# Kernel optimization log

Measured on AMD Instinct MI355X. Metric: run time of the kernel, lower is better.

## Reference

```python
import jax, jax.numpy as jnp
import numpy as np

N = 3000          # num_sample (nodes)
N_OMICS = 3000    # input feature dims for both omics
ENC1, ENC2, NZ = 256, 128, 64


def _xavier(key, fan_in, fan_out):
    limit = float(np.sqrt(6.0 / (fan_in + fan_out)))
    return jax.random.uniform(key, (fan_in, fan_out), jnp.float32, -limit, limit)


def setup_inputs() -> dict:
    key = jax.random.key(0)
    ks = jax.random.split(key, 20)
    inp = {
        "omics_1": jax.random.normal(ks[0], (N, N_OMICS), jnp.float32),
        "omics_2": jax.random.normal(ks[1], (N, N_OMICS), jnp.float32),
    }
    # random dense adjacency, row-normalized (as a typical normalized graph operator)
    for i, name in enumerate(["adj_feature_omics1", "adj_feature_omics2",
                              "adj_spatial_omics1", "adj_spatial_omics2"]):
        a = jax.random.uniform(ks[2 + i], (N, N), jnp.float32)
        inp[name] = a / jnp.sum(a, axis=1, keepdims=True)
    # GNNLayer weights for the four GAE encoders (xavier uniform, as in reset_parameters)
    dims = [(N_OMICS, ENC1), (ENC1, ENC2), (ENC2, NZ)]
    kidx = 6
    for enc in ["f1", "f2", "s1", "s2"]:
        for li, (fi, fo) in enumerate(dims, start=1):
            inp[f"w_{enc}_{li}"] = _xavier(ks[kidx], fi, fo)
            kidx += 1
    return inp


def _gae_encoder(x, adj, w1, w2, w3):
    # GNNLayer: support = act(x @ W); out = spmm(adj, support). Dropout is identity (eval).
    z = adj @ jnp.tanh(x @ w1)          # [N, ENC1]
    z = adj @ jnp.tanh(z @ w2)          # [N, ENC2]
    z = adj @ (z @ w3)                  # [N, NZ]  (no activation on layer 3)
    adj_hat = jax.nn.sigmoid(z @ z.T)   # [N, N]
    return z, adj_hat


def reference(omics_1, omics_2,
              adj_feature_omics1, adj_feature_omics2,
              adj_spatial_omics1, adj_spatial_omics2,
              w_f1_1, w_f1_2, w_f1_3,
              w_f2_1, w_f2_2, w_f2_3,
              w_s1_1, w_s1_2, w_s1_3,
              w_s2_1, w_s2_2, w_s2_3):
    _, a1 = _gae_encoder(omics_1, adj_feature_omics1, w_f1_1, w_f1_2, w_f1_3)
    _, a2 = _gae_encoder(omics_2, adj_feature_omics2, w_f2_1, w_f2_2, w_f2_3)
    _, a3 = _gae_encoder(omics_1, adj_spatial_omics1, w_s1_1, w_s1_2, w_s1_3)
    _, a4 = _gae_encoder(omics_2, adj_spatial_omics2, w_s2_1, w_s2_2, w_s2_3)
    # stacked reconstructed adjacencies from the four encoders [4, N, N]
    return jnp.stack([a1, a2, a3, a4], axis=0)
```

## Files before the change

kernel.cpp:

```cpp
#include <hip/hip_runtime.h>
#include <stdint.h>
#include <stddef.h>


typedef __attribute__((ext_vector_type(8))) _Float16 half8;
typedef __attribute__((ext_vector_type(4))) float f32x4;

#define PAD 3072
#define MR  3000
#define ADJ_STRIDE ((size_t)PAD * PAD)

static __device__ __forceinline__ void async_cp16(const _Float16* g, _Float16* l) {
    __builtin_amdgcn_global_load_lds((const __attribute__((address_space(1))) void*)g,
                                     (__attribute__((address_space(3))) void*)l, 16, 0, 0);
}

struct Adj4 { const float* src[4]; };

__global__ __launch_bounds__(256) void adj_cast4(Adj4 p, _Float16* __restrict__ dst) {
    const int z   = blockIdx.y;
    const int idx = blockIdx.x * 256 + threadIdx.x;
    const int row = idx / 192;
    const int u   = idx - row * 192;
    const int c0  = u * 16;
    const float* sp = p.src[z] + (size_t)row * MR + c0;
    _Float16* d = dst + (size_t)z * ADJ_STRIDE + (size_t)row * PAD + c0;
    half8 h0, h1;
    const bool rok = row < MR;
    if (rok && c0 < MR) {
        f32x4 v0 = __builtin_nontemporal_load((const f32x4*)sp);
        f32x4 v1 = __builtin_nontemporal_load((const f32x4*)(sp + 4));
        #pragma unroll
        for (int j = 0; j < 4; ++j) { h0[j] = (_Float16)v0[j]; h0[4 + j] = (_Float16)v1[j]; }
    } else {
        #pragma unroll
        for (int j = 0; j < 8; ++j) h0[j] = (_Float16)0.f;
    }
    if (rok && c0 + 8 < MR) {
        f32x4 v2 = __builtin_nontemporal_load((const f32x4*)(sp + 8));
        f32x4 v3 = __builtin_nontemporal_load((const f32x4*)(sp + 12));
        #pragma unroll
        for (int j = 0; j < 4; ++j) { h1[j] = (_Float16)v2[j]; h1[4 + j] = (_Float16)v3[j]; }
    } else {
        #pragma unroll
        for (int j = 0; j < 8; ++j) h1[j] = (_Float16)0.f;
    }
    *(half8*)d = h0;
    *(half8*)(d + 8) = h1;
}

struct Wt12 { const float* src[12]; _Float16* dst[12];
              int fi[12]; int fo[12]; int ldk[12]; int nr[12]; };

__global__ __launch_bounds__(256) void wt_cast12(Wt12 p) {
    const int z   = blockIdx.y;
    const int idx = blockIdx.x * 256 + threadIdx.x;
    const int ldk = p.ldk[z];
    if (idx >= p.nr[z] * ldk) return;
    const int r = idx / ldk;
    const int k = idx - r * ldk;
    float v = 0.f;
    if (r < p.fo[z] && k < p.fi[z]) v = p.src[z][(size_t)k * p.fo[z] + r];
    p.dst[z][(size_t)r * ldk + k] = (_Float16)v;
}

template<int ACT, int OMODE, int S, int BSRC>
__global__ __launch_bounds__(256, 2)
void gemm_bt(const _Float16* __restrict__ Aall, size_t aStride,
             const _Float16* __restrict__ Ball, size_t bStride,
             const float* __restrict__ Bf0, const float* __restrict__ Bf1,
             void* __restrict__ Call, size_t cStride,
             int M, int Ncols, int Kp, int lda, int ldb, int ldc,
             int mBound, int nBound)
{
    __shared__ _Float16 smem[128 * 64 * 2];
    _Float16* As = smem;
    _Float16* Bs = smem + 8192;

    const int z   = blockIdx.z;
    const int e   = z / S;
    const int ksl = z - e * S;
    const int Kslice = Kp / S;
    const int kbase  = ksl * Kslice;

    const _Float16* A = Aall + (size_t)e * aStride;
    const _Float16* B = Ball + (size_t)e * bStride;
    const float*    Bf = (e & 1) ? Bf1 : Bf0;

    const int tm = blockIdx.x * 128;
    const int tn = blockIdx.y * 128;
    const int t    = threadIdx.x;
    const int lane = t & 63;
    const int w    = t >> 6;
    const int wm   = (w >> 1) * 64;
    const int wn   = (w & 1) * 64;
    const int lr   = lane & 15;
    const int lg   = lane >> 4;

    f32x4 acc[4][4];
    const f32x4 zero = {0.f, 0.f, 0.f, 0.f};
    #pragma unroll
    for (int i = 0; i < 4; ++i)
        #pragma unroll
        for (int j = 0; j < 4; ++j) acc[i][j] = zero;

    const int nkt = Kslice >> 6;
    for (int kt = 0; kt < nkt; ++kt) {
        const int k0 = kbase + (kt << 6);
        #pragma unroll
        for (int i = 0; i < 4; ++i) {
            const int c = t + i * 256;
            const int row = c >> 3, slot = c & 7;
            const int ss = slot ^ (row & 7);
            async_cp16(A + (size_t)(tm + row) * lda + k0 + ss * 8, &As[c * 8]);
        }
        if (BSRC) {
            #pragma unroll
            for (int i = 0; i < 4; ++i) {
                const int c = t + i * 256;
                const int row = c >> 3, g = c & 7;
                const int grow = tn + row;
                const int gcol = k0 + g * 8;
                half8 h;
                if (grow < MR && gcol < MR) {
                    const float* bp = Bf + (size_t)grow * MR + gcol;
                    f32x4 v0 = *(const f32x4*)bp;
                    f32x4 v1 = *(const f32x4*)(bp + 4);
                    #pragma unroll
                    for (int j = 0; j < 4; ++j) { h[j] = (_Float16)v0[j]; h[4 + j] = (_Float16)v1[j]; }
                } else {
                    #pragma unroll
                    for (int j = 0; j < 8; ++j) h[j] = (_Float16)0.f;
                }
                *(half8*)&Bs[row * 64 + ((g ^ (row & 7)) << 3)] = h;
            }
        } else {
            #pragma unroll
            for (int i = 0; i < 4; ++i) {
                const int c = t + i * 256;
                const int row = c >> 3, slot = c & 7;
                const int ss = slot ^ (row & 7);
                async_cp16(B + (size_t)(tn + row) * ldb + k0 + ss * 8, &Bs[c * 8]);
            }
        }
        __syncthreads();

        #pragma unroll
        for (int ks = 0; ks < 2; ++ks) {
            half8 af[4], bf[4];
            #pragma unroll
            for (int mi = 0; mi < 4; ++mi) {
                const int ra = wm + mi * 16 + lr;
                const int s  = (ks * 4 + lg) ^ (ra & 7);
                af[mi] = *(const half8*)((const char*)As + ra * 128 + s * 16);
            }
            #pragma unroll
            for (int ni = 0; ni < 4; ++ni) {
                const int rb = wn + ni * 16 + lr;
                const int s  = (ks * 4 + lg) ^ (rb & 7);
                bf[ni] = *(const half8*)((const char*)Bs + rb * 128 + s * 16);
            }
            #pragma unroll
            for (int mi = 0; mi < 4; ++mi)
                #pragma unroll
                for (int ni = 0; ni < 4; ++ni)
                    acc[mi][ni] = __builtin_amdgcn_mfma_f32_16x16x32_f16(
                        af[mi], bf[ni], acc[mi][ni], 0, 0, 0);
        }
        __syncthreads();
    }

    if (OMODE == 0) {
        _Float16* C = (_Float16*)Call + (size_t)e * cStride;
        #pragma unroll
        for (int mi = 0; mi < 4; ++mi)
            #pragma unroll
            for (int rr = 0; rr < 4; ++rr) {
                const int m = tm + wm + mi * 16 + lg * 4 + rr;
                #pragma unroll
                for (int ni = 0; ni < 4; ++ni) {
                    const int n = tn + wn + ni * 16 + lr;
                    float x = acc[mi][ni][rr];
                    if (ACT) x = tanhf(x);
                    const bool ok = (m < M) && (n < Ncols);
                    C[(size_t)m * ldc + n] = ok ? (_Float16)x : (_Float16)0.f;
                }
            }
    } else {
        float* Cp = (float*)Call +
                    (size_t)(OMODE == 3 ? z : e) * cStride;
        float* ep = (float*)smem + w * 2048;
        #pragma unroll
        for (int hs = 0; hs < 2; ++hs) {
            __syncthreads();
            #pragma unroll
            for (int mi2 = 0; mi2 < 2; ++mi2)
                #pragma unroll
                for (int ni = 0; ni < 4; ++ni)
                    #pragma unroll
                    for (int rr = 0; rr < 4; ++rr) {
                        const int row = mi2 * 16 + lg * 4 + rr;
                        const int col = ni * 16 + lr;
                        const int sw  = (((row ^ (row >> 2)) & 3) << 4);
                        ep[row * 64 + (col ^ sw)] = acc[hs * 2 + mi2][ni][rr];
                    }
            __syncthreads();
            #pragma unroll
            for (int r2 = 0; r2 < 8; ++r2) {
                const int row = r2 * 4 + (lane >> 4);
                const int c4  = (lane & 15) * 4;
                const int sw  = (((row ^ (row >> 2)) & 3) << 4);
                f32x4 v = *(const f32x4*)&ep[row * 64 + (c4 ^ sw)];
                const int gm = tm + wm + hs * 32 + row;
                const int gn = tn + wn + c4;
                if (gm < mBound && gn < nBound) {
                    if (OMODE == 2) {
                        #pragma unroll
                        for (int j = 0; j < 4; ++j)
                            v[j] = 1.0f / (1.0f + __expf(-v[j]));
                    }
                    *(f32x4*)&Cp[(size_t)gm * ldc + gn] = v;
                }
            }
        }
    }
}

template<int ACT, int S>
__global__ __launch_bounds__(256)
void reduce_k(const float* __restrict__ P, _Float16* __restrict__ out, size_t region)
{
    const size_t e    = blockIdx.y;
    const size_t base = (size_t)(blockIdx.x * 256 + threadIdx.x) * 8;
    const float* p0 = P + e * S * region + base;
    f32x4 s0 = {0.f, 0.f, 0.f, 0.f}, s1 = s0;
    #pragma unroll
    for (int s = 0; s < S; ++s) {
        const float* p = p0 + (size_t)s * region;
        s0 += *(const f32x4*)p;
        s1 += *(const f32x4*)(p + 4);
    }
    half8 h;
    #pragma unroll
    for (int j = 0; j < 8; ++j) {
        float x = (j < 4) ? s0[j] : s1[j - 4];
        if (ACT) x = tanhf(x);
        h[j] = (_Float16)x;
    }
    *(half8*)(out + e * region + base) = h;
}

extern "C" void kernel_launch(void* const* d_in, const int* in_sizes, int n_in,
                              void* d_out, int out_size, void* d_ws, size_t ws_size,
                              hipStream_t stream)
{
    const float* X1 = (const float*)d_in[0];
    const float* X2 = (const float*)d_in[1];

    const size_t R1 = 786432;
    const size_t R2 = 393216;

    float* Part = (float*)d_ws;
    _Float16* hb = (_Float16*)(Part + 16 * R2);
    size_t off = 0;
    auto alloc = [&](size_t elems) { _Float16* p = hb + off; off += elems; return p; };
    _Float16* T1  = alloc(4 * R1);
    _Float16* Z1  = alloc(4 * R1);
    _Float16* T2  = alloc(4 * R2);
    _Float16* Z2  = alloc(4 * R2);
    _Float16* T3  = alloc(4 * R2);
    _Float16* Z3  = alloc(4 * R2);
    _Float16* W1t = alloc(4ull * 256 * PAD);
    _Float16* W2t = alloc(4ull * 128 * 256);
    _Float16* W3t = alloc(4ull * 128 * 128);
    _Float16* Adj = (_Float16*)d_out;

    Adj4 a4;
    for (int i = 0; i < 4; ++i) a4.src[i] = (const float*)d_in[2 + i];
    adj_cast4<<<dim3(2304, 4, 1), 256, 0, stream>>>(a4, Adj);

    Wt12 w12;
    for (int enc = 0; enc < 4; ++enc) {
        w12.src[enc]     = (const float*)d_in[6 + enc * 3 + 0];
        w12.dst[enc]     = W1t + (size_t)enc * 256 * PAD;
        w12.fi[enc] = MR;  w12.fo[enc] = 256; w12.ldk[enc] = PAD; w12.nr[enc] = 256;

        w12.src[4 + enc] = (const float*)d_in[6 + enc * 3 + 1];
        w12.dst[4 + enc] = W2t + (size_t)enc * 128 * 256;
        w12.fi[4 + enc] = 256; w12.fo[4 + enc] = 128; w12.ldk[4 + enc] = 256; w12.nr[4 + enc] = 128;

        w12.src[8 + enc] = (const float*)d_in[6 + enc * 3 + 2];
        w12.dst[8 + enc] = W3t + (size_t)enc * 128 * 128;
        w12.fi[8 + enc] = 128; w12.fo[8 + enc] = 64; w12.ldk[8 + enc] = 128; w12.nr[8 + enc] = 128;
    }
    wt_cast12<<<dim3(3072, 12, 1), 256, 0, stream>>>(w12);

    const int BIG = 1 << 30;

    gemm_bt<0, 3, 2, 1><<<dim3(2, 24, 8), 256, 0, stream>>>(
        W1t, (size_t)256 * PAD, nullptr, 0, X1, X2,
        Part, R1, 256, PAD, PAD, PAD, MR, PAD, BIG, BIG);
    reduce_k<1, 2><<<dim3(384, 4, 1), 256, 0, stream>>>(Part, T1, R1);

    gemm_bt<0, 3, 2, 0><<<dim3(24, 2, 8), 256, 0, stream>>>(
        Adj, ADJ_STRIDE, T1, R1, nullptr, nullptr,
        Part, R1, PAD, 256, PAD, PAD, PAD, 256, BIG, BIG);
    reduce_k<0, 2><<<dim3(384, 4, 1), 256, 0, stream>>>(Part, Z1, R1);

    gemm_bt<0, 3, 2, 0><<<dim3(1, 24, 8), 256, 0, stream>>>(
        W2t, (size_t)128 * 256, Z1, R1, nullptr, nullptr,
        Part, R2, 128, PAD, 256, 256, 256, PAD, BIG, BIG);
    reduce_k<1, 2><<<dim3(192, 4, 1), 256, 0, stream>>>(Part, T2, R2);

    gemm_bt<0, 3, 4, 0><<<dim3(24, 1, 16), 256, 0, stream>>>(
        Adj, ADJ_STRIDE, T2, R2, nullptr, nullptr,
        Part, R2, PAD, 128, PAD, PAD, PAD, 128, BIG, BIG);
    reduce_k<0, 4><<<dim3(192, 4, 1), 256, 0, stream>>>(Part, Z2, R2);

    gemm_bt<0, 0, 1, 0><<<dim3(1, 24, 4), 256, 0, stream>>>(
        W3t, (size_t)128 * 128, Z2, R2, nullptr, nullptr,
        T3, R2, 128, PAD, 128, 128, 128, PAD, BIG, BIG);

    gemm_bt<0, 3, 4, 0><<<dim3(24, 1, 16), 256, 0, stream>>>(
        Adj, ADJ_STRIDE, T3, R2, nullptr, nullptr,
        Part, R2, PAD, 128, PAD, PAD, PAD, 128, BIG, BIG);
    reduce_k<0, 4><<<dim3(192, 4, 1), 256, 0, stream>>>(Part, Z3, R2);

    gemm_bt<0, 2, 1, 0><<<dim3(24, 24, 4), 256, 0, stream>>>(
        Z3, R2, Z3, R2, nullptr, nullptr,
        d_out, (size_t)MR * MR, MR, MR, 128, 128, 128, MR, MR, MR);
}
```

Measured before the change: 312.1 us.

## Fuse adjacency cast into first GEMM launch, raise split-K, halve final K

The adjacency fp32-to-fp16 cast now runs as extra blocks inside the same launch as the first X·W1 GEMM, so the bandwidth-bound cast overlaps with compute instead of running as a separate kernel. Split-K factors rise (2→4 for the first two GEMMs, 4→8 for the two adjacency×128-wide GEMMs) to put more blocks on the device. The final Z·Zᵀ GEMM uses K=64 instead of the padded 128. The split-K partial buffer moves into the unused tail of the output buffer. The extra split-K slices add partial-sum traffic and reduction work in exchange for better occupancy.

New measurement: 274.4 us. -12.1%, faster.

```diff
diff --git a/kernel.cpp b/kernel.cpp
--- a/kernel.cpp
+++ b/kernel.cpp
@@ -13,40 +13,6 @@
 static __device__ __forceinline__ void async_cp16(const _Float16* g, _Float16* l) {
     __builtin_amdgcn_global_load_lds((const __attribute__((address_space(1))) void*)g,
                                      (__attribute__((address_space(3))) void*)l, 16, 0, 0);
-}
-
-struct Adj4 { const float* src[4]; };
-
-__global__ __launch_bounds__(256) void adj_cast4(Adj4 p, _Float16* __restrict__ dst) {
-    const int z   = blockIdx.y;
-    const int idx = blockIdx.x * 256 + threadIdx.x;
-    const int row = idx / 192;
-    const int u   = idx - row * 192;
-    const int c0  = u * 16;
-    const float* sp = p.src[z] + (size_t)row * MR + c0;
-    _Float16* d = dst + (size_t)z * ADJ_STRIDE + (size_t)row * PAD + c0;
-    half8 h0, h1;
-    const bool rok = row < MR;
-    if (rok && c0 < MR) {
-        f32x4 v0 = __builtin_nontemporal_load((const f32x4*)sp);
-        f32x4 v1 = __builtin_nontemporal_load((const f32x4*)(sp + 4));
-        #pragma unroll
-        for (int j = 0; j < 4; ++j) { h0[j] = (_Float16)v0[j]; h0[4 + j] = (_Float16)v1[j]; }
-    } else {
-        #pragma unroll
-        for (int j = 0; j < 8; ++j) h0[j] = (_Float16)0.f;
-    }
-    if (rok && c0 + 8 < MR) {
-        f32x4 v2 = __builtin_nontemporal_load((const f32x4*)(sp + 8));
-        f32x4 v3 = __builtin_nontemporal_load((const f32x4*)(sp + 12));
-        #pragma unroll
-        for (int j = 0; j < 4; ++j) { h1[j] = (_Float16)v2[j]; h1[4 + j] = (_Float16)v3[j]; }
-    } else {
-        #pragma unroll
-        for (int j = 0; j < 8; ++j) h1[j] = (_Float16)0.f;
-    }
-    *(half8*)d = h0;
-    *(half8*)(d + 8) = h1;
 }
 
 struct Wt12 { const float* src[12]; _Float16* dst[12];
@@ -64,31 +30,33 @@
     p.dst[z][(size_t)r * ldk + k] = (_Float16)v;
 }
 
+struct GArgs {
+    const _Float16* Aall; size_t aStride;
+    const _Float16* Ball; size_t bStride;
+    const float* Bf0; const float* Bf1;
+    void* Call; size_t cStride;
+    int M, Ncols, Kp, lda, ldb, ldc, mBound, nBound;
+};
+
 template<int ACT, int OMODE, int S, int BSRC>
-__global__ __launch_bounds__(256, 2)
-void gemm_bt(const _Float16* __restrict__ Aall, size_t aStride,
-             const _Float16* __restrict__ Ball, size_t bStride,
-             const float* __restrict__ Bf0, const float* __restrict__ Bf1,
-             void* __restrict__ Call, size_t cStride,
-             int M, int Ncols, int Kp, int lda, int ldb, int ldc,
-             int mBound, int nBound)
+static __device__ __forceinline__
+void gemm_body(const GArgs& ga, int bx, int by, int bz, _Float16* smem)
 {
-    __shared__ _Float16 smem[128 * 64 * 2];
     _Float16* As = smem;
     _Float16* Bs = smem + 8192;
 
-    const int z   = blockIdx.z;
+    const int z   = bz;
     const int e   = z / S;
     const int ksl = z - e * S;
-    const int Kslice = Kp / S;
+    const int Kslice = ga.Kp / S;
     const int kbase  = ksl * Kslice;
 
-    const _Float16* A = Aall + (size_t)e * aStride;
-    const _Float16* B = Ball + (size_t)e * bStride;
-    const float*    Bf = (e & 1) ? Bf1 : Bf0;
-
-    const int tm = blockIdx.x * 128;
-    const int tn = blockIdx.y * 128;
+    const _Float16* A = ga.Aall + (size_t)e * ga.aStride;
+    const _Float16* B = ga.Ball + (size_t)e * ga.bStride;
+    const float*    Bf = (e & 1) ? ga.Bf1 : ga.Bf0;
+
+    const int tm = bx * 128;
+    const int tn = by * 128;
     const int t    = threadIdx.x;
     const int lane = t & 63;
     const int w    = t >> 6;
@@ -112,7 +80,7 @@
             const int c = t + i * 256;
             const int row = c >> 3, slot = c & 7;
             const int ss = slot ^ (row & 7);
-            async_cp16(A + (size_t)(tm + row) * lda + k0 + ss * 8, &As[c * 8]);
+            async_cp16(A + (size_t)(tm + row) * ga.lda + k0 + ss * 8, &As[c * 8]);
         }
         if (BSRC) {
             #pragma unroll
@@ -140,7 +108,7 @@
                 const int c = t + i * 256;
                 const int row = c >> 3, slot = c & 7;
                 const int ss = slot ^ (row & 7);
-                async_cp16(B + (size_t)(tn + row) * ldb + k0 + ss * 8, &Bs[c * 8]);
+                async_cp16(B + (size_t)(tn + row) * ga.ldb + k0 + ss * 8, &Bs[c * 8]);
             }
         }
         __syncthreads();
@@ -171,7 +139,7 @@
     }
 
     if (OMODE == 0) {
-        _Float16* C = (_Float16*)Call + (size_t)e * cStride;
+        _Float16* C = (_Float16*)ga.Call + (size_t)e * ga.cStride;
         #pragma unroll
         for (int mi = 0; mi < 4; ++mi)
             #pragma unroll
@@ -182,13 +150,12 @@
                     const int n = tn + wn + ni * 16 + lr;
                     float x = acc[mi][ni][rr];
                     if (ACT) x = tanhf(x);
-                    const bool ok = (m < M) && (n < Ncols);
-                    C[(size_t)m * ldc + n] = ok ? (_Float16)x : (_Float16)0.f;
+                    const bool ok = (m < ga.M) && (n < ga.Ncols);
+                    C[(size_t)m * ga.ldc + n] = ok ? (_Float16)x : (_Float16)0.f;
                 }
             }
     } else {
-        float* Cp = (float*)Call +
-                    (size_t)(OMODE == 3 ? z : e) * cStride;
+        float* Cp = (float*)ga.Call + (size_t)(OMODE == 3 ? z : e) * ga.cStride;
         float* ep = (float*)smem + w * 2048;
         #pragma unroll
         for (int hs = 0; hs < 2; ++hs) {
@@ -213,16 +180,68 @@
                 f32x4 v = *(const f32x4*)&ep[row * 64 + (c4 ^ sw)];
                 const int gm = tm + wm + hs * 32 + row;
                 const int gn = tn + wn + c4;
-                if (gm < mBound && gn < nBound) {
+                if (gm < ga.mBound && gn < ga.nBound) {
                     if (OMODE == 2) {
                         #pragma unroll
                         for (int j = 0; j < 4; ++j)
                             v[j] = 1.0f / (1.0f + __expf(-v[j]));
                     }
-                    *(f32x4*)&Cp[(size_t)gm * ldc + gn] = v;
+                    *(f32x4*)&Cp[(size_t)gm * ga.ldc + gn] = v;
                 }
             }
         }
+    }
+}
+
+template<int ACT, int OMODE, int S, int BSRC>
+__global__ __launch_bounds__(256, 2)
+void gemm_bt(GArgs ga) {
+    __shared__ _Float16 smem[16384];
+    gemm_body<ACT, OMODE, S, BSRC>(ga, blockIdx.x, blockIdx.y, blockIdx.z, smem);
+}
+
+struct Adj4 { const float* src[4]; };
+
+__global__ __launch_bounds__(256, 2)
+void fused_s1(GArgs ga, Adj4 a4, _Float16* __restrict__ adst)
+{
+    __shared__ _Float16 smem[16384];
+    const int b = blockIdx.x;
+    if (b < 768) {
+        const int bz = b & 15;
+        const int r  = b >> 4;
+        gemm_body<0, 3, 4, 1>(ga, r & 1, r >> 1, bz, smem);
+    } else {
+        const int cb  = b - 768;
+        const int zz  = cb / 2304;
+        const int idx = (cb - zz * 2304) * 256 + threadIdx.x;
+        const int row = idx / 192;
+        const int u   = idx - row * 192;
+        const int c0  = u * 16;
+        const float* sp = a4.src[zz] + (size_t)row * MR + c0;
+        _Float16* d = adst + (size_t)zz * ADJ_STRIDE + (size_t)row * PAD + c0;
+        half8 h0, h1;
+        const bool rok = row < MR;
+        if (rok && c0 < MR) {
+            f32x4 v0 = __builtin_nontemporal_load((const f32x4*)sp);
+            f32x4 v1 = __builtin_nontemporal_load((const f32x4*)(sp + 4));
+            #pragma unroll
+            for (int j = 0; j < 4; ++j) { h0[j] = (_Float16)v0[j]; h0[4 + j] = (_Float16)v1[j]; }
+        } else {
+            #pragma unroll
+            for (int j = 0; j < 8; ++j) h0[j] = (_Float16)0.f;
+        }
+        if (rok && c0 + 8 < MR) {
+            f32x4 v2 = __builtin_nontemporal_load((const f32x4*)(sp + 8));
+            f32x4 v3 = __builtin_nontemporal_load((const f32x4*)(sp + 12));
+            #pragma unroll
+            for (int j = 0; j < 4; ++j) { h1[j] = (_Float16)v2[j]; h1[4 + j] = (_Float16)v3[j]; }
+        } else {
+            #pragma unroll
+            for (int j = 0; j < 8; ++j) h1[j] = (_Float16)0.f;
+        }
+        *(half8*)d = h0;
+        *(half8*)(d + 8) = h1;
     }
 }
 
@@ -260,8 +279,10 @@
     const size_t R1 = 786432;
     const size_t R2 = 393216;
 
-    float* Part = (float*)d_ws;
-    _Float16* hb = (_Float16*)(Part + 16 * R2);
+    _Float16* Adj  = (_Float16*)d_out;
+    float*    Part = (float*)(Adj + 4 * ADJ_STRIDE);
+
+    _Float16* hb = (_Float16*)d_ws;
     size_t off = 0;
     auto alloc = [&](size_t elems) { _Float16* p = hb + off; off += elems; return p; };
     _Float16* T1  = alloc(4 * R1);
@@ -273,11 +294,6 @@
     _Float16* W1t = alloc(4ull * 256 * PAD);
     _Float16* W2t = alloc(4ull * 128 * 256);
     _Float16* W3t = alloc(4ull * 128 * 128);
-    _Float16* Adj = (_Float16*)d_out;
-
-    Adj4 a4;
-    for (int i = 0; i < 4; ++i) a4.src[i] = (const float*)d_in[2 + i];
-    adj_cast4<<<dim3(2304, 4, 1), 256, 0, stream>>>(a4, Adj);
 
     Wt12 w12;
     for (int enc = 0; enc < 4; ++enc) {
@@ -297,36 +313,38 @@
 
     const int BIG = 1 << 30;
 
-    gemm_bt<0, 3, 2, 1><<<dim3(2, 24, 8), 256, 0, stream>>>(
-        W1t, (size_t)256 * PAD, nullptr, 0, X1, X2,
-        Part, R1, 256, PAD, PAD, PAD, MR, PAD, BIG, BIG);
-    reduce_k<1, 2><<<dim3(384, 4, 1), 256, 0, stream>>>(Part, T1, R1);
-
-    gemm_bt<0, 3, 2, 0><<<dim3(24, 2, 8), 256, 0, stream>>>(
-        Adj, ADJ_STRIDE, T1, R1, nullptr, nullptr,
-        Part, R1, PAD, 256, PAD, PAD, PAD, 256, BIG, BIG);
-    reduce_k<0, 2><<<dim3(384, 4, 1), 256, 0, stream>>>(Part, Z1, R1);
-
-    gemm_bt<0, 3, 2, 0><<<dim3(1, 24, 8), 256, 0, stream>>>(
-        W2t, (size_t)128 * 256, Z1, R1, nullptr, nullptr,
-        Part, R2, 128, PAD, 256, 256, 256, PAD, BIG, BIG);
+    GArgs g1 = { W1t, (size_t)256 * PAD, nullptr, 0, X1, X2,
+                 Part, R1, 256, PAD, PAD, PAD, MR, PAD, BIG, BIG };
+    Adj4 a4;
+    for (int i = 0; i < 4; ++i) a4.src[i] = (const float*)d_in[2 + i];
+    fused_s1<<<dim3(9984, 1, 1), 256, 0, stream>>>(g1, a4, Adj);
+    reduce_k<1, 4><<<dim3(384, 4, 1), 256, 0, stream>>>(Part, T1, R1);
+
+    GArgs g2 = { Adj, ADJ_STRIDE, T1, R1, nullptr, nullptr,
+                 Part, R1, PAD, 256, PAD, PAD, PAD, 256, BIG, BIG };
+    gemm_bt<0, 3, 4, 0><<<dim3(24, 2, 16), 256, 0, stream>>>(g2);
+    reduce_k<0, 4><<<dim3(384, 4, 1), 256, 0, stream>>>(Part, Z1, R1);
+
+    GArgs g3 = { W2t, (size_t)128 * 256, Z1, R1, nullptr, nullptr,
+                 Part, R2, 128, PAD, 256, 256, 256, PAD, BIG, BIG };
+    gemm_bt<0, 3, 2, 0><<<dim3(1, 24, 8), 256, 0, stream>>>(g3);
     reduce_k<1, 2><<<dim3(192, 4, 1), 256, 0, stream>>>(Part, T2, R2);
 
-    gemm_bt<0, 3, 4, 0><<<dim3(24, 1, 16), 256, 0, stream>>>(
-        Adj, ADJ_STRIDE, T2, R2, nullptr, nullptr,
-        Part, R2, PAD, 128, PAD, PAD, PAD, 128, BIG, BIG);
-    reduce_k<0, 4><<<dim3(192, 4, 1), 256, 0, stream>>>(Part, Z2, R2);
-
-    gemm_bt<0, 0, 1, 0><<<dim3(1, 24, 4), 256, 0, stream>>>(
-        W3t, (size_t)128 * 128, Z2, R2, nullptr, nullptr,
-        T3, R2, 128, PAD, 128, 128, 128, PAD, BIG, BIG);
-
-    gemm_bt<0, 3, 4, 0><<<dim3(24, 1, 16), 256, 0, stream>>>(
-        Adj, ADJ_STRIDE, T3, R2, nullptr, nullptr,
-        Part, R2, PAD, 128, PAD, PAD, PAD, 128, BIG, BIG);
-    reduce_k<0, 4><<<dim3(192, 4, 1), 256, 0, stream>>>(Part, Z3, R2);
-
-    gemm_bt<0, 2, 1, 0><<<dim3(24, 24, 4), 256, 0, stream>>>(
-        Z3, R2, Z3, R2, nullptr, nullptr,
-        d_out, (size_t)MR * MR, MR, MR, 128, 128, 128, MR, MR, MR);
-}
+    GArgs g4 = { Adj, ADJ_STRIDE, T2, R2, nullptr, nullptr,
+                 Part, R2, PAD, 128, PAD, PAD, PAD, 128, BIG, BIG };
+    gemm_bt<0, 3, 8, 0><<<dim3(24, 1, 32), 256, 0, stream>>>(g4);
+    reduce_k<0, 8><<<dim3(192, 4, 1), 256, 0, stream>>>(Part, Z2, R2);
+
+    GArgs g5 = { W3t, (size_t)128 * 128, Z2, R2, nullptr, nullptr,
+                 T3, R2, 128, PAD, 128, 128, 128, PAD, BIG, BIG };
+    gemm_bt<0, 0, 1, 0><<<dim3(1, 24, 4), 256, 0, stream>>>(g5);
+
+    GArgs g6 = { Adj, ADJ_STRIDE, T3, R2, nullptr, nullptr,
+                 Part, R2, PAD, 128, PAD, PAD, PAD, 128, BIG, BIG };
+    gemm_bt<0, 3, 8, 0><<<dim3(24, 1, 32), 256, 0, stream>>>(g6);
+    reduce_k<0, 8><<<dim3(192, 4, 1), 256, 0, stream>>>(Part, Z3, R2);
+
+    GArgs g7 = { Z3, R2, Z3, R2, nullptr, nullptr,
+                 d_out, (size_t)MR * MR, MR, MR, 64, 128, 128, MR, MR, MR };
+    gemm_bt<0, 2, 1, 0><<<dim3(24, 24, 4), 256, 0, stream>>>(g7);
+}
```
